# Performance work log

Hardware: AMD Instinct MI355X
Metric: run time of the kernel (lower is better)

Reference implementation:

```python
import jax, jax.numpy as jnp
import numpy as np

DIM = 4096
NUM_SHARDS = 8
BATCH, SEQ = 4, 4096


def setup_inputs() -> dict:
    key = jax.random.key(0)
    k1, k2 = jax.random.split(key)
    x = jax.random.normal(k1, (BATCH, SEQ, DIM), dtype=jnp.float32)
    # learned per-shard full-dim weight vectors (torch inits to zeros; use randn for a
    # non-degenerate correctness baseline)
    shards = jax.random.normal(k2, (NUM_SHARDS, DIM), dtype=jnp.float32)
    # contiguous block mapping of dims to shards, as in _init_shard_mapping
    dims_per_shard = DIM // NUM_SHARDS
    shard_map = jnp.minimum(jnp.arange(DIM) // dims_per_shard, NUM_SHARDS - 1).astype(jnp.int64)
    return {"x": x, "shards": shards, "shard_map": shard_map}


def reference(x, shards, shard_map):
    # Each dim d belongs to exactly one shard, so the masked multiply-accumulate
    # over shards collapses to a single per-dim gathered weight:
    #   out[..., d] = x[..., d] * shards[shard_map[d], d]
    w = shards[shard_map, jnp.arange(shards.shape[1])]  # [dim]
    return x * w
```

## Files before the change

### kernel.cpp

```cpp
#include <hip/hip_runtime.h>
#include <hip/hip_bf16.h>

#define DIM 4096
#define NUM_SHARDS 8
#define TOTAL_ELEMS (4 * 4096 * 4096)
#define TOTAL_F4 (TOTAL_ELEMS / 4)
#define DIM_F4 (DIM / 4)

__global__ void build_w_kernel(const float* __restrict__ shards,
                               const int* __restrict__ shard_map,
                               float* __restrict__ w) {
    int d = blockIdx.x * blockDim.x + threadIdx.x;
    if (d < DIM) {
        w[d] = shards[shard_map[d] * DIM + d];
    }
}

__global__ __launch_bounds__(256) void scale_kernel(const float4* __restrict__ x,
                                                    const float4* __restrict__ w,
                                                    float4* __restrict__ out) {
    int i = blockIdx.x * 256 + threadIdx.x;
    float4 xv = x[i];
    float4 wv = w[i & (DIM_F4 - 1)];
    float4 ov;
    ov.x = xv.x * wv.x;
    ov.y = xv.y * wv.y;
    ov.z = xv.z * wv.z;
    ov.w = xv.w * wv.w;
    out[i] = ov;
}

extern "C" void kernel_launch(void* const* d_in, const int* in_sizes, int n_in,
                              void* d_out, int out_size, void* d_ws, size_t ws_size,
                              hipStream_t stream) {
    const float* x = (const float*)d_in[0];
    const float* shards = (const float*)d_in[1];
    const int* shard_map = (const int*)d_in[2];
    float* w = (float*)d_ws;
    float* out = (float*)d_out;

    build_w_kernel<<<DIM / 256, 256, 0, stream>>>(shards, shard_map, w);

    scale_kernel<<<TOTAL_F4 / 256, 256, 0, stream>>>(
        (const float4*)x, (const float4*)w, (float4*)out);
}
```

Measured before the change: 420.3 us.

## Fuse weight gather into grid-stride scale kernel with nontemporal accesses

Removes the separate weight-building kernel and workspace by having each thread gather its four weights once. This works because the grid stride is a multiple of the row width, so a thread always sees the same columns. The main loop becomes a persistent grid-stride loop with nontemporal loads and stores to stream x and out past the cache. The trade-off is a fixed grid size that may underfill or constrain memory parallelism, plus redundant gathers of the weights across threads.

After: 450.2 us. 7.1% more time.

```diff
diff --git a/kernel.cpp b/kernel.cpp
--- a/kernel.cpp
+++ b/kernel.cpp
@@ -1,33 +1,38 @@
 #include <hip/hip_runtime.h>
-#include <hip/hip_bf16.h>
 
 #define DIM 4096
 #define NUM_SHARDS 8
 #define TOTAL_ELEMS (4 * 4096 * 4096)
 #define TOTAL_F4 (TOTAL_ELEMS / 4)
 #define DIM_F4 (DIM / 4)
+#define BLOCK 256
+#define GRID_BLOCKS 2048
 
-__global__ void build_w_kernel(const float* __restrict__ shards,
-                               const int* __restrict__ shard_map,
-                               float* __restrict__ w) {
-    int d = blockIdx.x * blockDim.x + threadIdx.x;
-    if (d < DIM) {
-        w[d] = shards[shard_map[d] * DIM + d];
+typedef float f4 __attribute__((ext_vector_type(4)));
+
+__global__ __launch_bounds__(BLOCK) void fused_scale_kernel(
+    const f4* __restrict__ x,
+    const float* __restrict__ shards,
+    const int* __restrict__ shard_map,
+    f4* __restrict__ out) {
+    const int tid = blockIdx.x * BLOCK + threadIdx.x;
+
+    const int c = tid & (DIM_F4 - 1);
+    const int d = c << 2;
+
+    f4 wv;
+    wv.x = shards[shard_map[d + 0] * DIM + (d + 0)];
+    wv.y = shards[shard_map[d + 1] * DIM + (d + 1)];
+    wv.z = shards[shard_map[d + 2] * DIM + (d + 2)];
+    wv.w = shards[shard_map[d + 3] * DIM + (d + 3)];
+
+    const int stride = GRID_BLOCKS * BLOCK;
+    #pragma unroll 4
+    for (int i = tid; i < TOTAL_F4; i += stride) {
+        f4 xv = __builtin_nontemporal_load(&x[i]);
+        f4 ov = xv * wv;
+        __builtin_nontemporal_store(ov, &out[i]);
     }
-}
-
-__global__ __launch_bounds__(256) void scale_kernel(const float4* __restrict__ x,
-                                                    const float4* __restrict__ w,
-                                                    float4* __restrict__ out) {
-    int i = blockIdx.x * 256 + threadIdx.x;
-    float4 xv = x[i];
-    float4 wv = w[i & (DIM_F4 - 1)];
-    float4 ov;
-    ov.x = xv.x * wv.x;
-    ov.y = xv.y * wv.y;
-    ov.z = xv.z * wv.z;
-    ov.w = xv.w * wv.w;
-    out[i] = ov;
 }
 
 extern "C" void kernel_launch(void* const* d_in, const int* in_sizes, int n_in,
@@ -36,11 +41,10 @@
     const float* x = (const float*)d_in[0];
     const float* shards = (const float*)d_in[1];
     const int* shard_map = (const int*)d_in[2];
-    float* w = (float*)d_ws;
     float* out = (float*)d_out;
 
-    build_w_kernel<<<DIM / 256, 256, 0, stream>>>(shards, shard_map, w);
+    (void)d_ws; (void)ws_size;
 
-    scale_kernel<<<TOTAL_F4 / 256, 256, 0, stream>>>(
-        (const float4*)x, (const float4*)w, (float4*)out);
+    fused_scale_kernel<<<GRID_BLOCKS, BLOCK, 0, stream>>>(
+        (const f4*)x, shards, shard_map, (f4*)out);
 }
```
